# Optimization experiments

Measured on AMD Instinct MI355X. Metric: run time of the kernel, lower is better.

Reference implementation:

```python
import jax, jax.numpy as jnp
import numpy as np

N = 50000
EH = 500000
ES = 250000
D_IN = 128
D_HID = 128
N_CLS = 47


def _mean_agg(feat, src, dst, n):
    # gather src features, scatter-mean onto dst (DGL copy_u + mean)
    msg = feat[src]                                   # [E, d]
    s = jax.ops.segment_sum(msg, dst, num_segments=n)  # [N, d]
    cnt = jax.ops.segment_sum(jnp.ones((src.shape[0],), feat.dtype), dst, num_segments=n)
    return s / jnp.maximum(cnt, 1.0)[:, None]


def _sage_cv_layer(H, HBar, W, b, hs, hd, ss, sd):
    hbar_new = _mean_agg(HBar, hs, hd, N)             # history etype
    hdelta_new = _mean_agg(H - HBar, ss, sd, N)       # sampled etype
    h_neigh = hbar_new + hdelta_new
    z = jnp.concatenate([H, h_neigh], axis=1)         # [N, 2*d_in]
    return jax.nn.relu(z @ W.T + b)


def setup_inputs() -> dict:
    key = jax.random.key(0)
    ks = jax.random.split(key, 16)
    gain = float(np.sqrt(2.0))  # calculate_gain('relu')

    def xavier(k, shape):
        fan_out, fan_in = shape
        a = gain * np.sqrt(6.0 / (fan_in + fan_out))
        return jax.random.uniform(k, shape, jnp.float32, -a, a)

    return {
        "x": jax.random.normal(ks[0], (N, D_IN), jnp.float32),
        "hbar0": jax.random.normal(ks[1], (N, D_IN), jnp.float32),
        "hbar1": jax.random.normal(ks[2], (N, D_HID), jnp.float32),
        "W0": xavier(ks[3], (D_HID, 2 * D_IN)),
        "b0": jnp.zeros((D_HID,), jnp.float32),
        "W1": xavier(ks[4], (N_CLS, 2 * D_HID)),
        "b1": jnp.zeros((N_CLS,), jnp.float32),
        "hist_src0": jax.random.randint(ks[5], (EH,), 0, N),
        "hist_dst0": jax.random.randint(ks[6], (EH,), 0, N),
        "samp_src0": jax.random.randint(ks[7], (ES,), 0, N),
        "samp_dst0": jax.random.randint(ks[8], (ES,), 0, N),
        "hist_src1": jax.random.randint(ks[9], (EH,), 0, N),
        "hist_dst1": jax.random.randint(ks[10], (EH,), 0, N),
        "samp_src1": jax.random.randint(ks[11], (ES,), 0, N),
        "samp_dst1": jax.random.randint(ks[12], (ES,), 0, N),
    }


def reference(x, hbar0, hbar1, W0, b0, W1, b1,
              hist_src0, hist_dst0, samp_src0, samp_dst0,
              hist_src1, hist_dst1, samp_src1, samp_dst1):
    h = _sage_cv_layer(x, hbar0, W0, b0, hist_src0, hist_dst0, samp_src0, samp_dst0)
    h = _sage_cv_layer(h, hbar1, W1, b1, hist_src1, hist_dst1, samp_src1, samp_dst1)
    return h  # [N, n_classes]
```

## Files before the change

### kernel.cpp

```cpp
#include <hip/hip_runtime.h>

#define D_FEAT 128
#define K_DIM  256
#define EPB 4096
#define PADL 136

typedef __attribute__((ext_vector_type(8))) short bf16x8;
typedef __attribute__((ext_vector_type(4))) float f32x4;

__device__ __forceinline__ unsigned short f2b(float f) {
    union { float f; unsigned u; } cv; cv.f = f;
    return (unsigned short)((cv.u + 0x7fffu + ((cv.u >> 16) & 1u)) >> 16);
}

__device__ __forceinline__ unsigned pack2(float lo, float hi) {
    return (unsigned)f2b(lo) | ((unsigned)f2b(hi) << 16);
}

__device__ __forceinline__ uint4 pack8(float4 a, float4 b) {
    return make_uint4(pack2(a.x, a.y), pack2(a.z, a.w), pack2(b.x, b.y), pack2(b.z, b.w));
}

__device__ __forceinline__ void addu4(float* a, uint4 v) {
    union { unsigned u; float f; } c;
    c.u = v.x << 16;         a[0] += c.f;
    c.u = v.x & 0xffff0000u; a[1] += c.f;
    c.u = v.y << 16;         a[2] += c.f;
    c.u = v.y & 0xffff0000u; a[3] += c.f;
    c.u = v.z << 16;         a[4] += c.f;
    c.u = v.z & 0xffff0000u; a[5] += c.f;
    c.u = v.w << 16;         a[6] += c.f;
    c.u = v.w & 0xffff0000u; a[7] += c.f;
}

__device__ __forceinline__ float blo(unsigned u) { union { unsigned u; float f; } c; c.u = u << 16; return c.f; }
__device__ __forceinline__ float bhi(unsigned u) { union { unsigned u; float f; } c; c.u = u & 0xffff0000u; return c.f; }

__device__ __forceinline__ long yoff(int y, int EH, int ES) {
    return (long)((y + 1) >> 1) * EH + (long)(y >> 1) * ES;
}


__global__ __launch_bounds__(256)
void histB(const int* __restrict__ hd0, const int* __restrict__ sd0,
           const int* __restrict__ hd1, const int* __restrict__ sd1,
           int EH, int ES, int* __restrict__ bucketCnt, int nb2) {
    int y = blockIdx.y;
    const int* d = (y == 0) ? hd0 : (y == 1) ? sd0 : (y == 2) ? hd1 : sd1;
    int E = (y & 1) ? ES : EH;
    __shared__ int cnt[256];
    int t = threadIdx.x;
    cnt[t] = 0;
    __syncthreads();
    int i0 = blockIdx.x * EPB;
    #pragma unroll
    for (int j = 0; j < 16; ++j) {
        int i = i0 + j * 256 + t;
        if (i < E) atomicAdd(&cnt[d[i] >> 8], 1);
    }
    __syncthreads();
    if (t < nb2 && cnt[t] > 0) atomicAdd(&bucketCnt[y * nb2 + t], cnt[t]);
}

__global__ __launch_bounds__(256)
void scanBuckets(const int* __restrict__ bucketCnt, int* __restrict__ rpBucket,
                 int* __restrict__ bcur, int nb2) {
    int y = blockIdx.x;
    int t = threadIdx.x;
    __shared__ int sh[256];
    int c = (t < nb2) ? bucketCnt[y * nb2 + t] : 0;
    sh[t] = c;
    __syncthreads();
    for (int o = 1; o < 256; o <<= 1) {
        int x = (t >= o) ? sh[t - o] : 0;
        __syncthreads();
        sh[t] += x;
        __syncthreads();
    }
    int excl = t ? sh[t - 1] : 0;
    if (t < nb2) {
        rpBucket[y * (nb2 + 1) + t] = excl;
        bcur[y * nb2 + t] = excl;
    }
    if (t == 0) rpBucket[y * (nb2 + 1) + nb2] = sh[255];
}

__global__ __launch_bounds__(256)
void binA(const int* __restrict__ hs0, const int* __restrict__ hd0,
          const int* __restrict__ ss0, const int* __restrict__ sd0,
          const int* __restrict__ hs1, const int* __restrict__ hd1,
          const int* __restrict__ ss1, const int* __restrict__ sd1,
          int EH, int ES, int* __restrict__ bcur, unsigned* __restrict__ recs,
          int nb2) {
    int y = blockIdx.y;
    const int* src = (y == 0) ? hs0 : (y == 1) ? ss0 : (y == 2) ? hs1 : ss1;
    const int* dst = (y == 0) ? hd0 : (y == 1) ? sd0 : (y == 2) ? hd1 : sd1;
    int E = (y & 1) ? ES : EH;
    unsigned* rb = recs + yoff(y, EH, ES);

    __shared__ int cnt[256];
    int t = threadIdx.x;
    cnt[t] = 0;
    __syncthreads();
    int i0 = blockIdx.x * EPB;
    #pragma unroll
    for (int j = 0; j < 16; ++j) {
        int i = i0 + j * 256 + t;
        if (i < E) atomicAdd(&cnt[dst[i] >> 8], 1);
    }
    __syncthreads();
    int c = cnt[t];
    __syncthreads();
    if (t < nb2 && c > 0) cnt[t] = atomicAdd(&bcur[y * nb2 + t], c);
    __syncthreads();
    #pragma unroll
    for (int j = 0; j < 16; ++j) {
        int i = i0 + j * 256 + t;
        if (i < E) {
            int dd = dst[i];
            int slot = atomicAdd(&cnt[dd >> 8], 1);
            rb[slot] = (unsigned)src[i] | ((unsigned)(dd & 255) << 24);
        }
    }
}

__global__ __launch_bounds__(256)
void placeB(const unsigned* __restrict__ recs, const int* __restrict__ rpBucket,
            int* __restrict__ rpAll, int* __restrict__ srcAll,
            int EH, int ES, int n, int nb2) {
    int y = blockIdx.y;
    int b = blockIdx.x;
    int E = (y & 1) ? ES : EH;
    int* rp = rpAll + (size_t)y * (n + 1);
    long off = yoff(y, EH, ES);
    const unsigned* rb = recs + off;
    int* sb = srcAll + off;
    int e0 = rpBucket[y * (nb2 + 1) + b];
    int e1 = rpBucket[y * (nb2 + 1) + b + 1];
    int nodeBase = b << 8;

    __shared__ int cnt[256];
    __shared__ int sh[256];
    int t = threadIdx.x;
    cnt[t] = 0;
    __syncthreads();
    for (int e = e0 + t; e < e1; e += 256)
        atomicAdd(&cnt[rb[e] >> 24], 1);
    __syncthreads();
    sh[t] = cnt[t];
    __syncthreads();
    for (int o = 1; o < 256; o <<= 1) {
        int x = (t >= o) ? sh[t - o] : 0;
        __syncthreads();
        sh[t] += x;
        __syncthreads();
    }
    int base = e0 + (t ? sh[t - 1] : 0);
    if (nodeBase + t < n) rp[nodeBase + t] = base;
    if (b == 0 && t == 0) rp[n] = E;
    cnt[t] = base;
    __syncthreads();
    for (int e = e0 + t; e < e1; e += 256) {
        unsigned r = rb[e];
        int p = atomicAdd(&cnt[r >> 24], 1);
        sb[p] = (int)(r & 0x00FFFFFFu);
    }
}

__global__ __launch_bounds__(256)
void prep_static(const float4* __restrict__ x, const float4* __restrict__ hbar0,
                 const float4* __restrict__ hbar1,
                 uint4* __restrict__ hb0, uint4* __restrict__ db0,
                 uint4* __restrict__ hb1, uint4* __restrict__ z, int n16) {
    int i = blockIdx.x * 256 + threadIdx.x;
    if (i >= n16) return;
    float4 xa = x[i * 2],     xb = x[i * 2 + 1];
    float4 ba = hbar0[i * 2], bb = hbar0[i * 2 + 1];
    float4 ca = hbar1[i * 2], cb = hbar1[i * 2 + 1];
    hb0[i] = pack8(ba, bb);
    db0[i] = pack8(make_float4(xa.x - ba.x, xa.y - ba.y, xa.z - ba.z, xa.w - ba.w),
                   make_float4(xb.x - bb.x, xb.y - bb.y, xb.z - bb.z, xb.w - bb.w));
    hb1[i] = pack8(ca, cb);
    int g = i >> 4, seg = i & 15;
    z[(size_t)g * 32 + seg] = pack8(xa, xb);
}

__global__ __launch_bounds__(256)
void conv_weights(const float* __restrict__ W0, unsigned short* __restrict__ Wb0,
                  const float* __restrict__ W1, unsigned short* __restrict__ Wb1) {
    int i = blockIdx.x * 256 + threadIdx.x;
    if (i < 128 * 256) Wb0[i] = f2b(W0[i]);
    if (i < 64 * 256) {
        int r = i >> 8;
        Wb1[i] = (r < 47) ? f2b(W1[i]) : (unsigned short)0;
    }
}

__global__ __launch_bounds__(256)
void aggregate_z(const uint4* __restrict__ HB, const uint4* __restrict__ DB,
                 const int* __restrict__ rpH, const int* __restrict__ srcH,
                 const int* __restrict__ rpS, const int* __restrict__ srcS,
                 uint4* __restrict__ z, int n) {
    int g = blockIdx.x * 4 + (threadIdx.x >> 6);
    if (g >= n) return;
    int lane = threadIdx.x & 63;
    int j = lane >> 4, l = lane & 15;

    int hb_ = rpH[g], he = rpH[g + 1];
    int sb  = rpS[g], se = rpS[g + 1];

    float a[8] = {0, 0, 0, 0, 0, 0, 0, 0};
    for (int e0 = hb_; e0 < he; e0 += 8) {
        int e1 = e0 + j, e2 = e0 + 4 + j;
        uint4 v1 = make_uint4(0, 0, 0, 0), v2 = make_uint4(0, 0, 0, 0);
        if (e1 < he) v1 = HB[(size_t)srcH[e1] * 16 + l];
        if (e2 < he) v2 = HB[(size_t)srcH[e2] * 16 + l];
        addu4(a, v1); addu4(a, v2);
    }
    float d[8] = {0, 0, 0, 0, 0, 0, 0, 0};
    for (int e0 = sb; e0 < se; e0 += 8) {
        int e1 = e0 + j, e2 = e0 + 4 + j;
        uint4 v1 = make_uint4(0, 0, 0, 0), v2 = make_uint4(0, 0, 0, 0);
        if (e1 < se) v1 = DB[(size_t)srcS[e1] * 16 + l];
        if (e2 < se) v2 = DB[(size_t)srcS[e2] * 16 + l];
        addu4(d, v1); addu4(d, v2);
    }

    float rH = 1.0f / fmaxf((float)(he - hb_), 1.0f);
    float rS = 1.0f / fmaxf((float)(se - sb), 1.0f);
    float s[8];
    #pragma unroll
    for (int i = 0; i < 8; ++i) {
        float v = a[i] * rH + d[i] * rS;
        v += __shfl_xor(v, 16);
        v += __shfl_xor(v, 32);
        s[i] = v;
    }
    if (j == 0) {
        uint4 rv = make_uint4(pack2(s[0], s[1]), pack2(s[2], s[3]),
                              pack2(s[4], s[5]), pack2(s[6], s[7]));
        z[(size_t)g * 32 + 16 + l] = rv;
    }
}

__global__ __launch_bounds__(256, 2)
void gemm_mfma_l0(const unsigned short* __restrict__ Z, const unsigned short* __restrict__ Wb,
                  const float* __restrict__ bias, const float* __restrict__ hbar1,
                  unsigned short* __restrict__ db1, unsigned short* __restrict__ zl, int n) {
    __shared__ unsigned short hl[32 * PADL];
    int tid  = threadIdx.x;
    int wave = tid >> 6;
    int lane = tid & 63;
    int rt = wave >> 1;
    int ch = wave & 1;
    int m0 = blockIdx.x * 32;
    int cl = lane & 15;
    int kq = lane >> 4;

    int mr = m0 + rt * 16 + cl;
    int mc = (mr < n) ? mr : (n - 1);

    const short* Zs = (const short*)Z;
    const short* Ws = (const short*)Wb;
    const short* aP = Zs + (size_t)mc * 256 + kq * 8;
    const short* bP = Ws + (size_t)(ch * 64 + cl) * 256 + kq * 8;

    bf16x8 aF[8];
    #pragma unroll
    for (int k0 = 0; k0 < 8; ++k0) aF[k0] = *(const bf16x8*)(aP + k0 * 32);

    f32x4 acc[4] = {};
    bf16x8 bF[2][4];
    #pragma unroll
    for (int t = 0; t < 4; ++t) bF[0][t] = *(const bf16x8*)(bP + t * 16 * 256);

    #pragma unroll
    for (int k0 = 0; k0 < 8; ++k0) {
        int cur = k0 & 1, nxt = cur ^ 1;
        if (k0 < 7) {
            int ko = (k0 + 1) * 32;
            #pragma unroll
            for (int t = 0; t < 4; ++t)
                bF[nxt][t] = *(const bf16x8*)(bP + t * 16 * 256 + ko);
        }
        #pragma unroll
        for (int t = 0; t < 4; ++t)
            acc[t] = __builtin_amdgcn_mfma_f32_16x16x32_bf16(aF[k0], bF[cur][t], acc[t], 0, 0, 0);
    }

    #pragma unroll
    for (int t = 0; t < 4; ++t) {
        int c = ch * 64 + t * 16 + cl;
        float bv = bias[c];
        #pragma unroll
        for (int r = 0; r < 4; ++r) {
            int row = rt * 16 + kq * 4 + r;
            hl[row * PADL + c] = f2b(fmaxf(acc[t][r] + bv, 0.0f));
        }
    }
    __syncthreads();

    int row  = tid >> 3;
    int col  = (tid & 7) * 16;
    int m    = m0 + row;
    if (m < n) {
        const uint4* hr = (const uint4*)(hl + row * PADL + col);
        uint4 v0 = hr[0];
        uint4 v1 = hr[1];
        uint4* zp = (uint4*)(zl + (size_t)m * 256 + col);
        zp[0] = v0;
        zp[1] = v1;
        const float4* hb = (const float4*)(hbar1 + (size_t)m * 128 + col);
        float4 h0 = hb[0], h1 = hb[1], h2 = hb[2], h3 = hb[3];
        uint4 d0, d1;
        d0.x = pack2(blo(v0.x) - h0.x, bhi(v0.x) - h0.y);
        d0.y = pack2(blo(v0.y) - h0.z, bhi(v0.y) - h0.w);
        d0.z = pack2(blo(v0.z) - h1.x, bhi(v0.z) - h1.y);
        d0.w = pack2(blo(v0.w) - h1.z, bhi(v0.w) - h1.w);
        d1.x = pack2(blo(v1.x) - h2.x, bhi(v1.x) - h2.y);
        d1.y = pack2(blo(v1.y) - h2.z, bhi(v1.y) - h2.w);
        d1.z = pack2(blo(v1.z) - h3.x, bhi(v1.z) - h3.y);
        d1.w = pack2(blo(v1.w) - h3.z, bhi(v1.w) - h3.w);
        uint4* dp = (uint4*)(db1 + (size_t)m * 128 + col);
        dp[0] = d0;
        dp[1] = d1;
    }
}

template<int NT>
__global__ __launch_bounds__(128, 2)
void gemm_mfma(const unsigned short* __restrict__ Z, const unsigned short* __restrict__ Wb,
               const float* __restrict__ bias, float* __restrict__ out, int n, int COLS) {
    int wave = threadIdx.x >> 6;
    int lane = threadIdx.x & 63;
    int m0 = blockIdx.x * 32 + wave * 16;
    int cl = lane & 15;
    int kq = lane >> 4;
    int mr = m0 + cl;
    int mc = (mr < n) ? mr : (n - 1);

    const short* Zs = (const short*)Z;
    const short* Ws = (const short*)Wb;
    const short* aP = Zs + (size_t)mc * 256 + kq * 8;
    const short* bP = Ws + (size_t)cl * 256 + kq * 8;

    bf16x8 aF[8];
    #pragma unroll
    for (int k0 = 0; k0 < 8; ++k0) aF[k0] = *(const bf16x8*)(aP + k0 * 32);

    f32x4 acc[NT] = {};
    bf16x8 bF[2][NT];
    #pragma unroll
    for (int t = 0; t < NT; ++t) bF[0][t] = *(const bf16x8*)(bP + t * 16 * 256);

    #pragma unroll
    for (int k0 = 0; k0 < 8; ++k0) {
        int cur = k0 & 1, nxt = cur ^ 1;
        if (k0 < 7) {
            int ko = (k0 + 1) * 32;
            #pragma unroll
            for (int t = 0; t < NT; ++t)
                bF[nxt][t] = *(const bf16x8*)(bP + t * 16 * 256 + ko);
        }
        #pragma unroll
        for (int t = 0; t < NT; ++t)
            acc[t] = __builtin_amdgcn_mfma_f32_16x16x32_bf16(aF[k0], bF[cur][t], acc[t], 0, 0, 0);
    }

    int rg = kq * 4;
    #pragma unroll
    for (int t = 0; t < NT; ++t) {
        int c = t * 16 + cl;
        if (c >= COLS) continue;
        float bv = bias[c];
        #pragma unroll
        for (int r = 0; r < 4; ++r) {
            int m = m0 + rg + r;
            if (m < n) out[(size_t)m * COLS + c] = fmaxf(acc[t][r] + bv, 0.f);
        }
    }
}

extern "C" void kernel_launch(void* const* d_in, const int* in_sizes, int n_in,
                              void* d_out, int out_size, void* d_ws, size_t ws_size,
                              hipStream_t stream) {
    const float* x     = (const float*)d_in[0];
    const float* hbar0 = (const float*)d_in[1];
    const float* hbar1 = (const float*)d_in[2];
    const float* W0    = (const float*)d_in[3];
    const float* b0    = (const float*)d_in[4];
    const float* W1    = (const float*)d_in[5];
    const float* b1    = (const float*)d_in[6];
    const int* hs0 = (const int*)d_in[7];
    const int* hd0 = (const int*)d_in[8];
    const int* ss0 = (const int*)d_in[9];
    const int* sd0 = (const int*)d_in[10];
    const int* hs1 = (const int*)d_in[11];
    const int* hd1 = (const int*)d_in[12];
    const int* ss1 = (const int*)d_in[13];
    const int* sd1 = (const int*)d_in[14];

    const int n   = in_sizes[0] / D_FEAT;
    const int EH  = in_sizes[7];
    const int ES  = in_sizes[9];
    const int nb2 = (n + 255) / 256;

    int* bucketCnt = (int*)d_ws;
    int* rpBucket  = bucketCnt + 4 * nb2;
    int* bcur      = rpBucket + 4 * (nb2 + 1);
    int* rpAll     = bcur + 4 * nb2;
    int* srcAll    = rpAll + 4 * (size_t)(n + 1);
    unsigned* recs = (unsigned*)(srcAll + 2 * (size_t)EH + 2 * (size_t)ES);
    size_t int_words = (size_t)12 * nb2 + 4 + 4 * (size_t)(n + 1)
                     + 4 * (size_t)EH + 4 * (size_t)ES;
    int_words = (int_words + 3) & ~(size_t)3;
    unsigned short* hb0 = (unsigned short*)((int*)d_ws + int_words);
    unsigned short* db0 = hb0 + (size_t)n * D_FEAT;
    unsigned short* hb1 = db0 + (size_t)n * D_FEAT;
    unsigned short* db1 = hb1 + (size_t)n * D_FEAT;
    unsigned short* z   = db1 + (size_t)n * D_FEAT;
    unsigned short* Wb0 = z + (size_t)n * K_DIM;
    unsigned short* Wb1 = Wb0 + 128 * 256;

    const int* rpH0 = rpAll;
    const int* rpS0 = rpAll + (size_t)(n + 1);
    const int* rpH1 = rpAll + 2 * (size_t)(n + 1);
    const int* rpS1 = rpAll + 3 * (size_t)(n + 1);
    int* srcH0 = srcAll;
    int* srcS0 = srcAll + (size_t)EH;
    int* srcH1 = srcAll + (size_t)EH + ES;
    int* srcS1 = srcAll + 2 * (size_t)EH + ES;

    dim3 blk(256);
    int binb  = (EH + EPB - 1) / EPB;
    int prepb = ((n * 16) + 255) / 256;
    int aggb  = (n + 3) / 4;
    int gemmb0 = (n + 31) / 32;
    int gemmb1 = (n + 31) / 32;

    hipMemsetAsync(bucketCnt, 0, 4 * (size_t)nb2 * sizeof(int), stream);
    conv_weights<<<128, blk, 0, stream>>>(W0, Wb0, W1, Wb1);
    histB<<<dim3(binb, 4), blk, 0, stream>>>(hd0, sd0, hd1, sd1, EH, ES, bucketCnt, nb2);
    scanBuckets<<<4, blk, 0, stream>>>(bucketCnt, rpBucket, bcur, nb2);
    binA<<<dim3(binb, 4), blk, 0, stream>>>(hs0, hd0, ss0, sd0, hs1, hd1, ss1, sd1,
                                            EH, ES, bcur, recs, nb2);
    placeB<<<dim3(nb2, 4), blk, 0, stream>>>(recs, rpBucket, rpAll, srcAll, EH, ES, n, nb2);
    prep_static<<<prepb, blk, 0, stream>>>((const float4*)x, (const float4*)hbar0,
                                           (const float4*)hbar1, (uint4*)hb0, (uint4*)db0,
                                           (uint4*)hb1, (uint4*)z, n * 16);

    aggregate_z<<<aggb, blk, 0, stream>>>((const uint4*)hb0, (const uint4*)db0,
                                          rpH0, srcH0, rpS0, srcS0, (uint4*)z, n);
    gemm_mfma_l0<<<gemmb0, blk, 0, stream>>>(z, Wb0, b0, hbar1, db1, z, n);

    aggregate_z<<<aggb, blk, 0, stream>>>((const uint4*)hb1, (const uint4*)db1,
                                          rpH1, srcH1, rpS1, srcS1, (uint4*)z, n);
    gemm_mfma<3><<<gemmb1, dim3(128), 0, stream>>>(z, Wb1, b1, (float*)d_out, n, 47);
}
```

Measured before the change: 331.7 us.

## Store Z and weights in MFMA fragment-major layout for coalesced GEMM loads

The concatenated Z matrix and both bf16 weight matrices are now stored in a tiled fragment order, grouped in 16-row blocks by k-step and lane. Each wave's A and B fragment loads then become contiguous 1KB reads instead of strided 512-byte row accesses. The producers (prep_static, aggregate_z, gemm_mfma_l0's LDS writeback, conv_weights) are rewritten to emit this layout. Buffer padding for the last partial 16-row group is added, at the cost of more complex scattered writes in the producers.

```diff
diff --git a/kernel.cpp b/kernel.cpp
--- a/kernel.cpp
+++ b/kernel.cpp
@@ -4,6 +4,7 @@
 #define K_DIM  256
 #define EPB 4096
 #define PADL 136
+
 
 typedef __attribute__((ext_vector_type(8))) short bf16x8;
 typedef __attribute__((ext_vector_type(4))) float f32x4;
@@ -182,17 +183,32 @@
                    make_float4(xb.x - bb.x, xb.y - bb.y, xb.z - bb.z, xb.w - bb.w));
     hb1[i] = pack8(ca, cb);
     int g = i >> 4, seg = i & 15;
-    z[(size_t)g * 32 + seg] = pack8(xa, xb);
-}
-
-__global__ __launch_bounds__(256)
-void conv_weights(const float* __restrict__ W0, unsigned short* __restrict__ Wb0,
-                  const float* __restrict__ W1, unsigned short* __restrict__ Wb1) {
+    int G = g >> 4, r = g & 15, k0 = seg >> 2, kq = seg & 3;
+    z[((size_t)G * 8 + k0) * 64 + kq * 16 + r] = pack8(xa, xb);
+}
+
+__global__ __launch_bounds__(256)
+void conv_weights(const float* __restrict__ W0, unsigned short* __restrict__ WbF0,
+                  const float* __restrict__ W1, unsigned short* __restrict__ WbF1) {
     int i = blockIdx.x * 256 + threadIdx.x;
-    if (i < 128 * 256) Wb0[i] = f2b(W0[i]);
-    if (i < 64 * 256) {
-        int r = i >> 8;
-        Wb1[i] = (r < 47) ? f2b(W1[i]) : (unsigned short)0;
+    if (i < 4096) {
+        int k0 = i >> 9, T = (i >> 6) & 7, lane = i & 63;
+        int col = T * 16 + (lane & 15);
+        int kb = k0 * 32 + (lane >> 4) * 8;
+        const float* src = W0 + (size_t)col * 256 + kb;
+        unsigned short* dst = WbF0 + (size_t)i * 8;
+        #pragma unroll
+        for (int e = 0; e < 8; ++e) dst[e] = f2b(src[e]);
+    }
+    if (i < 1536) {
+        int k0 = i / 192, rem = i % 192;
+        int T = rem >> 6, lane = rem & 63;
+        int col = T * 16 + (lane & 15);
+        int kb = k0 * 32 + (lane >> 4) * 8;
+        unsigned short* dst = WbF1 + (size_t)i * 8;
+        #pragma unroll
+        for (int e = 0; e < 8; ++e)
+            dst[e] = (col < 47) ? f2b(W1[(size_t)col * 256 + kb + e]) : (unsigned short)0;
     }
 }
 
@@ -239,7 +255,8 @@
     if (j == 0) {
         uint4 rv = make_uint4(pack2(s[0], s[1]), pack2(s[2], s[3]),
                               pack2(s[4], s[5]), pack2(s[6], s[7]));
-        z[(size_t)g * 32 + 16 + l] = rv;
+        size_t slot = ((size_t)(g >> 4) * 8 + 4 + (l >> 2)) * 64 + (l & 3) * 16 + (g & 15);
+        z[slot] = rv;
     }
 }
 
@@ -257,31 +274,28 @@
     int cl = lane & 15;
     int kq = lane >> 4;
 
-    int mr = m0 + rt * 16 + cl;
-    int mc = (mr < n) ? mr : (n - 1);
-
-    const short* Zs = (const short*)Z;
-    const short* Ws = (const short*)Wb;
-    const short* aP = Zs + (size_t)mc * 256 + kq * 8;
-    const short* bP = Ws + (size_t)(ch * 64 + cl) * 256 + kq * 8;
+    const short* Af = (const short*)Z;
+    const short* Bf = (const short*)Wb;
+    size_t G = (size_t)(m0 >> 4) + rt;
 
     bf16x8 aF[8];
     #pragma unroll
-    for (int k0 = 0; k0 < 8; ++k0) aF[k0] = *(const bf16x8*)(aP + k0 * 32);
+    for (int k0 = 0; k0 < 8; ++k0)
+        aF[k0] = *(const bf16x8*)(Af + ((G * 8 + k0) * 64 + lane) * 8);
 
     f32x4 acc[4] = {};
     bf16x8 bF[2][4];
     #pragma unroll
-    for (int t = 0; t < 4; ++t) bF[0][t] = *(const bf16x8*)(bP + t * 16 * 256);
+    for (int t = 0; t < 4; ++t)
+        bF[0][t] = *(const bf16x8*)(Bf + ((size_t)((0 * 8 + ch * 4 + t)) * 64 + lane) * 8);
 
     #pragma unroll
     for (int k0 = 0; k0 < 8; ++k0) {
         int cur = k0 & 1, nxt = cur ^ 1;
         if (k0 < 7) {
-            int ko = (k0 + 1) * 32;
             #pragma unroll
             for (int t = 0; t < 4; ++t)
-                bF[nxt][t] = *(const bf16x8*)(bP + t * 16 * 256 + ko);
+                bF[nxt][t] = *(const bf16x8*)(Bf + ((size_t)(((k0 + 1) * 8 + ch * 4 + t)) * 64 + lane) * 8);
         }
         #pragma unroll
         for (int t = 0; t < 4; ++t)
@@ -299,6 +313,19 @@
         }
     }
     __syncthreads();
+
+    #pragma unroll
+    for (int s = 0; s < 2; ++s) {
+        int ls = tid + s * 256;
+        int gi = ls >> 8, k0 = (ls >> 6) & 3, ln = ls & 63;
+        int rl = gi * 16 + (ln & 15);
+        int col = k0 * 32 + (ln >> 4) * 8;
+        int m = m0 + rl;
+        if (m < n) {
+            uint4 v = *(const uint4*)(hl + rl * PADL + col);
+            ((uint4*)zl)[((size_t)(m0 >> 4) + gi) * 8 * 64 + (size_t)k0 * 64 + ln] = v;
+        }
+    }
 
     int row  = tid >> 3;
     int col  = (tid & 7) * 16;
@@ -307,9 +334,6 @@
         const uint4* hr = (const uint4*)(hl + row * PADL + col);
         uint4 v0 = hr[0];
         uint4 v1 = hr[1];
-        uint4* zp = (uint4*)(zl + (size_t)m * 256 + col);
-        zp[0] = v0;
-        zp[1] = v1;
         const float4* hb = (const float4*)(hbar1 + (size_t)m * 128 + col);
         float4 h0 = hb[0], h1 = hb[1], h2 = hb[2], h3 = hb[3];
         uint4 d0, d1;
@@ -336,31 +360,29 @@
     int m0 = blockIdx.x * 32 + wave * 16;
     int cl = lane & 15;
     int kq = lane >> 4;
-    int mr = m0 + cl;
-    int mc = (mr < n) ? mr : (n - 1);
-
-    const short* Zs = (const short*)Z;
-    const short* Ws = (const short*)Wb;
-    const short* aP = Zs + (size_t)mc * 256 + kq * 8;
-    const short* bP = Ws + (size_t)cl * 256 + kq * 8;
+
+    const short* Af = (const short*)Z;
+    const short* Bf = (const short*)Wb;
+    size_t G = (size_t)(m0 >> 4);
 
     bf16x8 aF[8];
     #pragma unroll
-    for (int k0 = 0; k0 < 8; ++k0) aF[k0] = *(const bf16x8*)(aP + k0 * 32);
+    for (int k0 = 0; k0 < 8; ++k0)
+        aF[k0] = *(const bf16x8*)(Af + ((G * 8 + k0) * 64 + lane) * 8);
 
     f32x4 acc[NT] = {};
     bf16x8 bF[2][NT];
     #pragma unroll
-    for (int t = 0; t < NT; ++t) bF[0][t] = *(const bf16x8*)(bP + t * 16 * 256);
+    for (int t = 0; t < NT; ++t)
+        bF[0][t] = *(const bf16x8*)(Bf + ((size_t)(0 * NT + t) * 64 + lane) * 8);
 
     #pragma unroll
     for (int k0 = 0; k0 < 8; ++k0) {
         int cur = k0 & 1, nxt = cur ^ 1;
         if (k0 < 7) {
-            int ko = (k0 + 1) * 32;
             #pragma unroll
             for (int t = 0; t < NT; ++t)
-                bF[nxt][t] = *(const bf16x8*)(bP + t * 16 * 256 + ko);
+                bF[nxt][t] = *(const bf16x8*)(Bf + ((size_t)((k0 + 1) * NT + t) * 64 + lane) * 8);
         }
         #pragma unroll
         for (int t = 0; t < NT; ++t)
@@ -419,7 +441,7 @@
     unsigned short* hb1 = db0 + (size_t)n * D_FEAT;
     unsigned short* db1 = hb1 + (size_t)n * D_FEAT;
     unsigned short* z   = db1 + (size_t)n * D_FEAT;
-    unsigned short* Wb0 = z + (size_t)n * K_DIM;
+    unsigned short* Wb0 = z + (size_t)n * K_DIM + 4096;
     unsigned short* Wb1 = Wb0 + 128 * 256;
 
     const int* rpH0 = rpAll;
@@ -439,7 +461,7 @@
     int gemmb1 = (n + 31) / 32;
 
     hipMemsetAsync(bucketCnt, 0, 4 * (size_t)nb2 * sizeof(int), stream);
-    conv_weights<<<128, blk, 0, stream>>>(W0, Wb0, W1, Wb1);
+    conv_weights<<<16, blk, 0, stream>>>(W0, Wb0, W1, Wb1);
     histB<<<dim3(binb, 4), blk, 0, stream>>>(hd0, sd0, hd1, sd1, EH, ES, bucketCnt, nb2);
     scanBuckets<<<4, blk, 0, stream>>>(bucketCnt, rpBucket, bcur, nb2);
     binA<<<dim3(binb, 4), blk, 0, stream>>>(hs0, hd0, ss0, sd0, hs1, hd1, ss1, sd1,
```

Result: faster. 305.1 us (-8.0%).
